# Performance work log

Hardware: AMD Instinct MI355X
Metric: run time of the kernel (lower is better)

Reference implementation:

```python
import jax, jax.numpy as jnp
import numpy as np

H, N, CH = 256, 64, 1  # heads/features, diagonal state size, channels


def setup_inputs() -> dict:
    key = jax.random.key(0)
    k1, k2, k3 = jax.random.split(key, 3)
    # |A| in (0.5, 0.999) so exp(dtA * l) decays for large l (matches rho*w construction)
    A_abslog = jnp.log(jax.random.uniform(k1, (H, N), dtype=jnp.float32,
                                          minval=0.5, maxval=0.999))
    A_phase = jax.random.uniform(k2, (H, N), dtype=jnp.float32,
                                 minval=-np.pi, maxval=np.pi)
    # C stored as real view of complex (channels, H, N, 2), like torch.view_as_real
    C = jax.random.normal(k3, (CH, H, N, 2), dtype=jnp.float32)
    return {"A_abslog": A_abslog, "A_phase": A_phase, "C": C, "L": 4096}


def reference(A_abslog, A_phase, C, L):
    # A_eigvals = exp(abslog + i*phase), copies=1 so repeat is identity
    A = jnp.exp(A_abslog + 1j * A_phase)            # (H, N) complex64
    dtA = jnp.log(A)                                 # (H, N)
    Cc = C[..., 0] + 1j * C[..., 1]                  # (CH, H, N)
    Cc = Cc * (A - 1.0) / dtA                        # (CH, H, N)
    t = jnp.arange(L, dtype=jnp.float32)             # (L,)
    K = jnp.exp(dtA[:, :, None] * t)                 # (H, N, L) Vandermonde
    K = jnp.einsum('chn,hnl->chl', Cc, K)            # (CH, H, L)
    return 2.0 * K.real
```

## Files before the change

kernel.cpp:

```cpp
#include <hip/hip_runtime.h>
#include <math.h>


typedef _Float16 f16x8 __attribute__((ext_vector_type(8)));
typedef float    f32x4 __attribute__((ext_vector_type(4)));

constexpr int H = 256;
constexpr int N = 64;
constexpr int L = 4096;

__global__ void sskdiag_kernel(const float* __restrict__ A_abslog,
                               const float* __restrict__ A_phase,
                               const float* __restrict__ C,
                               float* __restrict__ out)
{
    __shared__ float4 s_tabA[N];
    __shared__ float4 s_tabB[N];

    const int h    = blockIdx.x;
    const int lane = threadIdx.x;

    {
        const int n = lane;
        const float al = A_abslog[h * N + n];
        const float ph = A_phase [h * N + n];
        const double md = (double)ph * 0.15915494309189535;
        const float phrev = (float)(md - floor(md));
        const float sp = __builtin_amdgcn_sinf(phrev);
        const float cp = __builtin_amdgcn_cosf(phrev);
        const float m  = __expf(al);
        const float Ar = m * cp, Ai = m * sp;
        const float nr = Ar - 1.0f, ni = Ai;
        const float inv = 1.0f / (al * al + ph * ph);
        const float gr = (nr * al + ni * ph) * inv;
        const float gi = (ni * al - nr * ph) * inv;
        const float cre = C[(h * N + n) * 2 + 0];
        const float cim = C[(h * N + n) * 2 + 1];
        const float Cr = 2.0f * (cre * gr - cim * gi);
        const float Ci = 2.0f * (cre * gi + cim * gr);
        const double m16 = 16.0 * md, m1024 = 1024.0 * md;
        const float f16a  = (float)(m16   - floor(m16));
        const float f1024 = (float)(m1024 - floor(m1024));
        const float mg16   = __expf(16.0f * al);
        const float mg1024 = __expf(1024.0f * al);
        s_tabA[n] = make_float4(al, phrev, Cr, Ci);
        s_tabB[n] = make_float4(mg16   * __builtin_amdgcn_cosf(f16a),
                                mg16   * __builtin_amdgcn_sinf(f16a),
                                mg1024 * __builtin_amdgcn_cosf(f1024),
                                mg1024 * __builtin_amdgcn_sinf(f1024));
    }
    __syncthreads();

    const int e  = lane & 15;
    const int kg = lane >> 4;

    f16x8 fGr[2][4], fGi[2][4], fMr[2][4], fMi[2][4];

    #pragma unroll
    for (int s = 0; s < 2; ++s) {
        #pragma unroll
        for (int j = 0; j < 8; ++j) {
            const int n = 32 * s + 8 * kg + j;
            const float4 tA = s_tabA[n];
            const float4 tB = s_tabB[n];
            float tg = tA.y * (float)e;  tg -= floorf(tg);
            const float magg = __expf(tA.x * (float)e);
            float gr_ = magg * __builtin_amdgcn_cosf(tg);
            float gi_ = magg * __builtin_amdgcn_sinf(tg);
            float tm = tA.y * (float)(64 * e);  tm -= floorf(tm);
            const float magm = __expf(tA.x * (float)(64 * e));
            const float ur = magm * __builtin_amdgcn_cosf(tm);
            const float ui = magm * __builtin_amdgcn_sinf(tm);
            float mr_ = tA.z * ur - tA.w * ui;
            float mi_ = tA.z * ui + tA.w * ur;
            #pragma unroll
            for (int tt = 0; tt < 4; ++tt) {
                fGr[s][tt][j] = (_Float16)gr_;
                fGi[s][tt][j] = (_Float16)(-gi_);
                fMr[s][tt][j] = (_Float16)mr_;
                fMi[s][tt][j] = (_Float16)mi_;
                if (tt < 3) {
                    const float ngr = gr_ * tB.x - gi_ * tB.y;
                    gi_ = gr_ * tB.y + gi_ * tB.x;  gr_ = ngr;
                    const float nmr = mr_ * tB.z - mi_ * tB.w;
                    mi_ = mr_ * tB.w + mi_ * tB.z;  mr_ = nmr;
                }
            }
        }
    }

    #pragma unroll
    for (int ta = 0; ta < 4; ++ta) {
        #pragma unroll
        for (int tb = 0; tb < 4; ++tb) {
            f32x4 acc = {0.f, 0.f, 0.f, 0.f};
            #pragma unroll
            for (int s = 0; s < 2; ++s) {
                acc = __builtin_amdgcn_mfma_f32_16x16x32_f16(fGr[s][tb], fMr[s][ta], acc, 0, 0, 0);
                acc = __builtin_amdgcn_mfma_f32_16x16x32_f16(fGi[s][tb], fMi[s][ta], acc, 0, 0, 0);
            }
            const int a  = ta * 16 + e;
            float4 v;
            v.x = acc[0];  v.y = acc[1];  v.z = acc[2];  v.w = acc[3];
            *reinterpret_cast<float4*>(out + h * L + a * 64 + tb * 16 + kg * 4) = v;
        }
    }
}

extern "C" void kernel_launch(void* const* d_in, const int* in_sizes, int n_in,
                              void* d_out, int out_size, void* d_ws, size_t ws_size,
                              hipStream_t stream)
{
    const float* A_abslog = (const float*)d_in[0];
    const float* A_phase  = (const float*)d_in[1];
    const float* C        = (const float*)d_in[2];
    float* out = (float*)d_out;

    sskdiag_kernel<<<H, 64, 0, stream>>>(A_abslog, A_phase, C, out);
}
```

Baseline: 11.42 us.

## Use four waves per head with shared-memory Vandermonde tables feeding MFMA

```diff
diff --git a/kernel.cpp b/kernel.cpp
--- a/kernel.cpp
+++ b/kernel.cpp
@@ -3,25 +3,31 @@
 
 
 typedef _Float16 f16x8 __attribute__((ext_vector_type(8)));
-typedef float    f32x4 __attribute__((ext_vector_type(4)));
+typedef unsigned short u16x8 __attribute__((ext_vector_type(8)));
+typedef unsigned int   u32x4 __attribute__((ext_vector_type(4)));
+typedef float          f32x4 __attribute__((ext_vector_type(4)));
 
 constexpr int H = 256;
 constexpr int N = 64;
 constexpr int L = 4096;
+constexpr int STRIDE = 76;
 
-__global__ void sskdiag_kernel(const float* __restrict__ A_abslog,
-                               const float* __restrict__ A_phase,
-                               const float* __restrict__ C,
-                               float* __restrict__ out)
+__global__ __launch_bounds__(256)
+void sskdiag_kernel(const float* __restrict__ A_abslog,
+                    const float* __restrict__ A_phase,
+                    const float* __restrict__ C,
+                    float* __restrict__ out)
 {
-    __shared__ float4 s_tabA[N];
-    __shared__ float4 s_tabB[N];
+    __shared__ float4   s_t1[N];
+    __shared__ float4   s_t2[N];
+    __shared__ unsigned s_G[64 * STRIDE];
+    __shared__ unsigned s_M[64 * STRIDE];
 
-    const int h    = blockIdx.x;
-    const int lane = threadIdx.x;
+    const int h   = blockIdx.x;
+    const int tid = threadIdx.x;
 
-    {
-        const int n = lane;
+    if (tid < N) {
+        const int n = tid;
         const float al = A_abslog[h * N + n];
         const float ph = A_phase [h * N + n];
         const double md = (double)ph * 0.15915494309189535;
@@ -38,72 +44,105 @@
         const float cim = C[(h * N + n) * 2 + 1];
         const float Cr = 2.0f * (cre * gr - cim * gi);
         const float Ci = 2.0f * (cre * gi + cim * gr);
-        const double m16 = 16.0 * md, m1024 = 1024.0 * md;
-        const float f16a  = (float)(m16   - floor(m16));
-        const float f1024 = (float)(m1024 - floor(m1024));
-        const float mg16   = __expf(16.0f * al);
-        const float mg1024 = __expf(1024.0f * al);
-        s_tabA[n] = make_float4(al, phrev, Cr, Ci);
-        s_tabB[n] = make_float4(mg16   * __builtin_amdgcn_cosf(f16a),
-                                mg16   * __builtin_amdgcn_sinf(f16a),
-                                mg1024 * __builtin_amdgcn_cosf(f1024),
-                                mg1024 * __builtin_amdgcn_sinf(f1024));
+        const double m64 = 64.0 * md;
+        const float f64a = (float)(m64 - floor(m64));
+        const float mg64 = __expf(64.0f * al);
+        s_t1[n] = make_float4(al, phrev, Ar, Ai);
+        s_t2[n] = make_float4(mg64 * __builtin_amdgcn_cosf(f64a),
+                              mg64 * __builtin_amdgcn_sinf(f64a), Cr, Ci);
     }
     __syncthreads();
 
-    const int e  = lane & 15;
-    const int kg = lane >> 4;
+    {
+        const int n = tid & 63, q = tid >> 6;
+        const float4 t1 = s_t1[n];
+        const float4 t2 = s_t2[n];
+        const float al = t1.x, phrev = t1.y;
+        const float Ar = t1.z, Ai = t1.w;
+        const float Ur = t2.x, Ui = t2.y;
+        const float b0 = (float)(16 * q);
+        float tg = phrev * b0;  tg -= floorf(tg);
+        const float gmag = __expf(al * b0);
+        float gre = gmag * __builtin_amdgcn_cosf(tg);
+        float gim = gmag * __builtin_amdgcn_sinf(tg);
+        const float a64 = (float)(1024 * q);
+        float tm = phrev * a64;  tm -= floorf(tm);
+        const float umag = __expf(al * a64);
+        const float ure = umag * __builtin_amdgcn_cosf(tm);
+        const float uim = umag * __builtin_amdgcn_sinf(tm);
+        float mre = t2.z * ure - t2.w * uim;
+        float mim = t2.z * uim + t2.w * ure;
 
-    f16x8 fGr[2][4], fGi[2][4], fMr[2][4], fMi[2][4];
+        #pragma unroll
+        for (int k = 0; k < 16; ++k) {
+            const int row = 16 * q + k;
+            union { _Float16 hh[2]; unsigned u; } pg, pm;
+            pg.hh[0] = (_Float16)gre;  pg.hh[1] = (_Float16)(-gim);
+            pm.hh[0] = (_Float16)mre;  pm.hh[1] = (_Float16)mim;
+            s_G[row * STRIDE + n] = pg.u;
+            s_M[row * STRIDE + n] = pm.u;
+            const float ngr = gre * Ar - gim * Ai;
+            gim = gre * Ai + gim * Ar;  gre = ngr;
+            const float nmr = mre * Ur - mim * Ui;
+            mim = mre * Ui + mim * Ur;  mre = nmr;
+        }
+    }
+    __syncthreads();
+
+    const int w    = tid >> 6;
+    const int lane = tid & 63;
+    const int e    = lane & 15;
+    const int kg   = lane >> 4;
+
+    f16x8 fGr[2][4], fGi[2][4], fMr[2], fMi[2];
 
     #pragma unroll
     for (int s = 0; s < 2; ++s) {
         #pragma unroll
-        for (int j = 0; j < 8; ++j) {
-            const int n = 32 * s + 8 * kg + j;
-            const float4 tA = s_tabA[n];
-            const float4 tB = s_tabB[n];
-            float tg = tA.y * (float)e;  tg -= floorf(tg);
-            const float magg = __expf(tA.x * (float)e);
-            float gr_ = magg * __builtin_amdgcn_cosf(tg);
-            float gi_ = magg * __builtin_amdgcn_sinf(tg);
-            float tm = tA.y * (float)(64 * e);  tm -= floorf(tm);
-            const float magm = __expf(tA.x * (float)(64 * e));
-            const float ur = magm * __builtin_amdgcn_cosf(tm);
-            const float ui = magm * __builtin_amdgcn_sinf(tm);
-            float mr_ = tA.z * ur - tA.w * ui;
-            float mi_ = tA.z * ui + tA.w * ur;
+        for (int tb = 0; tb < 4; ++tb) {
+            const unsigned* p = &s_G[(tb * 16 + e) * STRIDE + 32 * s + 8 * kg];
+            const u32x4 v0 = *reinterpret_cast<const u32x4*>(p);
+            const u32x4 v1 = *reinterpret_cast<const u32x4*>(p + 4);
+            u16x8 rr, ii;
             #pragma unroll
-            for (int tt = 0; tt < 4; ++tt) {
-                fGr[s][tt][j] = (_Float16)gr_;
-                fGi[s][tt][j] = (_Float16)(-gi_);
-                fMr[s][tt][j] = (_Float16)mr_;
-                fMi[s][tt][j] = (_Float16)mi_;
-                if (tt < 3) {
-                    const float ngr = gr_ * tB.x - gi_ * tB.y;
-                    gi_ = gr_ * tB.y + gi_ * tB.x;  gr_ = ngr;
-                    const float nmr = mr_ * tB.z - mi_ * tB.w;
-                    mi_ = mr_ * tB.w + mi_ * tB.z;  mr_ = nmr;
-                }
+            for (int k = 0; k < 4; ++k) {
+                rr[k]     = (unsigned short)(v0[k] & 0xffffu);
+                ii[k]     = (unsigned short)(v0[k] >> 16);
+                rr[k + 4] = (unsigned short)(v1[k] & 0xffffu);
+                ii[k + 4] = (unsigned short)(v1[k] >> 16);
             }
+            fGr[s][tb] = __builtin_bit_cast(f16x8, rr);
+            fGi[s][tb] = __builtin_bit_cast(f16x8, ii);
+        }
+        {
+            const unsigned* p = &s_M[(w * 16 + e) * STRIDE + 32 * s + 8 * kg];
+            const u32x4 v0 = *reinterpret_cast<const u32x4*>(p);
+            const u32x4 v1 = *reinterpret_cast<const u32x4*>(p + 4);
+            u16x8 rr, ii;
+            #pragma unroll
+            for (int k = 0; k < 4; ++k) {
+                rr[k]     = (unsigned short)(v0[k] & 0xffffu);
+                ii[k]     = (unsigned short)(v0[k] >> 16);
+                rr[k + 4] = (unsigned short)(v1[k] & 0xffffu);
+                ii[k + 4] = (unsigned short)(v1[k] >> 16);
+            }
+            fMr[s] = __builtin_bit_cast(f16x8, rr);
+            fMi[s] = __builtin_bit_cast(f16x8, ii);
         }
     }
 
     #pragma unroll
-    for (int ta = 0; ta < 4; ++ta) {
+    for (int tb = 0; tb < 4; ++tb) {
+        f32x4 acc = {0.f, 0.f, 0.f, 0.f};
         #pragma unroll
-        for (int tb = 0; tb < 4; ++tb) {
-            f32x4 acc = {0.f, 0.f, 0.f, 0.f};
-            #pragma unroll
-            for (int s = 0; s < 2; ++s) {
-                acc = __builtin_amdgcn_mfma_f32_16x16x32_f16(fGr[s][tb], fMr[s][ta], acc, 0, 0, 0);
-                acc = __builtin_amdgcn_mfma_f32_16x16x32_f16(fGi[s][tb], fMi[s][ta], acc, 0, 0, 0);
-            }
-            const int a  = ta * 16 + e;
-            float4 v;
-            v.x = acc[0];  v.y = acc[1];  v.z = acc[2];  v.w = acc[3];
-            *reinterpret_cast<float4*>(out + h * L + a * 64 + tb * 16 + kg * 4) = v;
+        for (int s = 0; s < 2; ++s) {
+            acc = __builtin_amdgcn_mfma_f32_16x16x32_f16(fGr[s][tb], fMr[s], acc, 0, 0, 0);
+            acc = __builtin_amdgcn_mfma_f32_16x16x32_f16(fGi[s][tb], fMi[s], acc, 0, 0, 0);
         }
+        const int a = w * 16 + e;
+        float4 v;
+        v.x = acc[0];  v.y = acc[1];  v.z = acc[2];  v.w = acc[3];
+        *reinterpret_cast<float4*>(out + h * L + a * 64 + tb * 16 + kg * 4) = v;
     }
 }
 
@@ -116,5 +155,5 @@
     const float* C        = (const float*)d_in[2];
     float* out = (float*)d_out;
 
-    sskdiag_kernel<<<H, 64, 0, stream>>>(A_abslog, A_phase, C, out);
+    sskdiag_kernel<<<H, 256, 0, stream>>>(A_abslog, A_phase, C, out);
 }
```

Measured after the change: 9.782 us. 14.4% less time.

## Use four waves per head and build fp16 Vandermonde tiles in swizzled LDS

Applied to the files above, without the earlier changes.

```diff
diff --git a/kernel.cpp b/kernel.cpp
--- a/kernel.cpp
+++ b/kernel.cpp
@@ -9,101 +9,120 @@
 constexpr int N = 64;
 constexpr int L = 4096;
 
-__global__ void sskdiag_kernel(const float* __restrict__ A_abslog,
-                               const float* __restrict__ A_phase,
-                               const float* __restrict__ C,
-                               float* __restrict__ out)
+__global__ __launch_bounds__(256)
+void sskdiag_kernel(const float* __restrict__ A_abslog,
+                    const float* __restrict__ A_phase,
+                    const float* __restrict__ C,
+                    float* __restrict__ out)
 {
-    __shared__ float4 s_tabA[N];
-    __shared__ float4 s_tabB[N];
+    __shared__ __align__(16) unsigned s_Gr[64 * 32], s_Gi[64 * 32];
+    __shared__ __align__(16) unsigned s_Mr[64 * 32], s_Mi[64 * 32];
 
-    const int h    = blockIdx.x;
-    const int lane = threadIdx.x;
+    const int h   = blockIdx.x;
+    const int tid = threadIdx.x;
+    const int n2  = tid & 31;
+    const int q   = tid >> 5;
 
-    {
-        const int n = lane;
-        const float al = A_abslog[h * N + n];
-        const float ph = A_phase [h * N + n];
+    const float2 alv = *reinterpret_cast<const float2*>(&A_abslog[h * N + 2 * n2]);
+    const float2 phv = *reinterpret_cast<const float2*>(&A_phase [h * N + 2 * n2]);
+    const float4 cv  = *reinterpret_cast<const float4*>(&C[(h * N + 2 * n2) * 2]);
+
+    float Ar[2], Ai[2], Ur[2], Ui[2];
+    float g_re[2], g_im[2], m_re[2], m_im[2];
+
+    #pragma unroll
+    for (int t = 0; t < 2; ++t) {
+        const float al = t ? alv.y : alv.x;
+        const float ph = t ? phv.y : phv.x;
         const double md = (double)ph * 0.15915494309189535;
         const float phrev = (float)(md - floor(md));
         const float sp = __builtin_amdgcn_sinf(phrev);
         const float cp = __builtin_amdgcn_cosf(phrev);
-        const float m  = __expf(al);
-        const float Ar = m * cp, Ai = m * sp;
-        const float nr = Ar - 1.0f, ni = Ai;
+        const float ma = __expf(al);
+        Ar[t] = ma * cp;  Ai[t] = ma * sp;
+        const float nr = Ar[t] - 1.0f, ni = Ai[t];
         const float inv = 1.0f / (al * al + ph * ph);
         const float gr = (nr * al + ni * ph) * inv;
         const float gi = (ni * al - nr * ph) * inv;
-        const float cre = C[(h * N + n) * 2 + 0];
-        const float cim = C[(h * N + n) * 2 + 1];
+        const float cre = t ? cv.z : cv.x;
+        const float cim = t ? cv.w : cv.y;
         const float Cr = 2.0f * (cre * gr - cim * gi);
         const float Ci = 2.0f * (cre * gi + cim * gr);
-        const double m16 = 16.0 * md, m1024 = 1024.0 * md;
-        const float f16a  = (float)(m16   - floor(m16));
-        const float f1024 = (float)(m1024 - floor(m1024));
-        const float mg16   = __expf(16.0f * al);
-        const float mg1024 = __expf(1024.0f * al);
-        s_tabA[n] = make_float4(al, phrev, Cr, Ci);
-        s_tabB[n] = make_float4(mg16   * __builtin_amdgcn_cosf(f16a),
-                                mg16   * __builtin_amdgcn_sinf(f16a),
-                                mg1024 * __builtin_amdgcn_cosf(f1024),
-                                mg1024 * __builtin_amdgcn_sinf(f1024));
+        const double m64 = 64.0 * md;
+        const float f64a = (float)(m64 - floor(m64));
+        const float mg64 = __expf(64.0f * al);
+        Ur[t] = mg64 * __builtin_amdgcn_cosf(f64a);
+        Ui[t] = mg64 * __builtin_amdgcn_sinf(f64a);
+        const float b0 = (float)(8 * q);
+        float tg = phrev * b0;  tg -= floorf(tg);
+        const float gm = __expf(al * b0);
+        g_re[t] = gm * __builtin_amdgcn_cosf(tg);
+        g_im[t] = gm * __builtin_amdgcn_sinf(tg);
+        const float e0 = (float)(512 * q);
+        float tm = phrev * e0;  tm -= floorf(tm);
+        const float um = __expf(al * e0);
+        const float ur = um * __builtin_amdgcn_cosf(tm);
+        const float ui = um * __builtin_amdgcn_sinf(tm);
+        m_re[t] = Cr * ur - Ci * ui;
+        m_im[t] = Cr * ui + Ci * ur;
+    }
+
+    #pragma unroll
+    for (int k = 0; k < 8; ++k) {
+        const int row  = 8 * q + k;
+        const int scol = (((n2 >> 2) ^ (row & 7)) << 2) | (n2 & 3);
+        const int idx  = row * 32 + scol;
+        s_Gr[idx] = __builtin_bit_cast(unsigned,
+                        __builtin_amdgcn_cvt_pkrtz(g_re[0], g_re[1]));
+        s_Gi[idx] = __builtin_bit_cast(unsigned,
+                        __builtin_amdgcn_cvt_pkrtz(-g_im[0], -g_im[1]));
+        s_Mr[idx] = __builtin_bit_cast(unsigned,
+                        __builtin_amdgcn_cvt_pkrtz(m_re[0], m_re[1]));
+        s_Mi[idx] = __builtin_bit_cast(unsigned,
+                        __builtin_amdgcn_cvt_pkrtz(m_im[0], m_im[1]));
+        #pragma unroll
+        for (int t = 0; t < 2; ++t) {
+            const float ng = g_re[t] * Ar[t] - g_im[t] * Ai[t];
+            g_im[t] = g_re[t] * Ai[t] + g_im[t] * Ar[t];  g_re[t] = ng;
+            const float nm = m_re[t] * Ur[t] - m_im[t] * Ui[t];
+            m_im[t] = m_re[t] * Ui[t] + m_im[t] * Ur[t];  m_re[t] = nm;
+        }
     }
     __syncthreads();
 
-    const int e  = lane & 15;
-    const int kg = lane >> 4;
+    const int w    = tid >> 6;
+    const int lane = tid & 63;
+    const int e    = lane & 15;
+    const int kg   = lane >> 4;
 
-    f16x8 fGr[2][4], fGi[2][4], fMr[2][4], fMi[2][4];
-
+    f16x8 fMr[2], fMi[2], fGr[2][4], fGi[2][4];
     #pragma unroll
     for (int s = 0; s < 2; ++s) {
+        const int rowm = w * 16 + e;
+        const int cm   = rowm * 32 + (((4 * s + kg) ^ (rowm & 7)) << 2);
+        fMr[s] = *reinterpret_cast<const f16x8*>(&s_Mr[cm]);
+        fMi[s] = *reinterpret_cast<const f16x8*>(&s_Mi[cm]);
         #pragma unroll
-        for (int j = 0; j < 8; ++j) {
-            const int n = 32 * s + 8 * kg + j;
-            const float4 tA = s_tabA[n];
-            const float4 tB = s_tabB[n];
-            float tg = tA.y * (float)e;  tg -= floorf(tg);
-            const float magg = __expf(tA.x * (float)e);
-            float gr_ = magg * __builtin_amdgcn_cosf(tg);
-            float gi_ = magg * __builtin_amdgcn_sinf(tg);
-            float tm = tA.y * (float)(64 * e);  tm -= floorf(tm);
-            const float magm = __expf(tA.x * (float)(64 * e));
-            const float ur = magm * __builtin_amdgcn_cosf(tm);
-            const float ui = magm * __builtin_amdgcn_sinf(tm);
-            float mr_ = tA.z * ur - tA.w * ui;
-            float mi_ = tA.z * ui + tA.w * ur;
-            #pragma unroll
-            for (int tt = 0; tt < 4; ++tt) {
-                fGr[s][tt][j] = (_Float16)gr_;
-                fGi[s][tt][j] = (_Float16)(-gi_);
-                fMr[s][tt][j] = (_Float16)mr_;
-                fMi[s][tt][j] = (_Float16)mi_;
-                if (tt < 3) {
-                    const float ngr = gr_ * tB.x - gi_ * tB.y;
-                    gi_ = gr_ * tB.y + gi_ * tB.x;  gr_ = ngr;
-                    const float nmr = mr_ * tB.z - mi_ * tB.w;
-                    mi_ = mr_ * tB.w + mi_ * tB.z;  mr_ = nmr;
-                }
-            }
+        for (int tb = 0; tb < 4; ++tb) {
+            const int rowg = tb * 16 + e;
+            const int cg   = rowg * 32 + (((4 * s + kg) ^ (rowg & 7)) << 2);
+            fGr[s][tb] = *reinterpret_cast<const f16x8*>(&s_Gr[cg]);
+            fGi[s][tb] = *reinterpret_cast<const f16x8*>(&s_Gi[cg]);
         }
     }
 
     #pragma unroll
-    for (int ta = 0; ta < 4; ++ta) {
+    for (int tb = 0; tb < 4; ++tb) {
+        f32x4 acc = {0.f, 0.f, 0.f, 0.f};
         #pragma unroll
-        for (int tb = 0; tb < 4; ++tb) {
-            f32x4 acc = {0.f, 0.f, 0.f, 0.f};
-            #pragma unroll
-            for (int s = 0; s < 2; ++s) {
-                acc = __builtin_amdgcn_mfma_f32_16x16x32_f16(fGr[s][tb], fMr[s][ta], acc, 0, 0, 0);
-                acc = __builtin_amdgcn_mfma_f32_16x16x32_f16(fGi[s][tb], fMi[s][ta], acc, 0, 0, 0);
-            }
-            const int a  = ta * 16 + e;
-            float4 v;
-            v.x = acc[0];  v.y = acc[1];  v.z = acc[2];  v.w = acc[3];
-            *reinterpret_cast<float4*>(out + h * L + a * 64 + tb * 16 + kg * 4) = v;
+        for (int s = 0; s < 2; ++s) {
+            acc = __builtin_amdgcn_mfma_f32_16x16x32_f16(fGr[s][tb], fMr[s], acc, 0, 0, 0);
+            acc = __builtin_amdgcn_mfma_f32_16x16x32_f16(fGi[s][tb], fMi[s], acc, 0, 0, 0);
         }
+        float4 v;
+        v.x = acc[0];  v.y = acc[1];  v.z = acc[2];  v.w = acc[3];
+        *reinterpret_cast<float4*>(out + h * L + (w * 16 + e) * 64
+                                   + tb * 16 + kg * 4) = v;
     }
 }
 
@@ -116,5 +135,5 @@
     const float* C        = (const float*)d_in[2];
     float* out = (float*)d_out;
 
-    sskdiag_kernel<<<H, 64, 0, stream>>>(A_abslog, A_phase, C, out);
+    sskdiag_kernel<<<H, 256, 0, stream>>>(A_abslog, A_phase, C, out);
 }
```

Result: slower. 14.88 us (+30.2%).
